# Kernel tuning notes

Measured on AMD Instinct MI355X. Metric: run time of the kernel, lower is better.

## Reference

```python
import jax, jax.numpy as jnp
import numpy as np
import math

def setup_inputs() -> dict:
    key = jax.random.key(0)
    k1, k2, k3 = jax.random.split(key, 3)
    B, N, C = 32, 1024, 768
    x = jax.random.normal(k1, (B, N, C), dtype=jnp.float32)
    W = jax.random.normal(k2, (4, C), dtype=jnp.float32) * 0.02  # conv1x1 weight [out=4, in=C]
    b = jax.random.normal(k3, (4,), dtype=jnp.float32) * 0.02
    return {"x": x, "W": W, "b": b}

def reference(x, W, b):
    B, N, C = x.shape
    H = int(math.isqrt(N))
    L = H * H
    # [B,N,C] -> [B,C,H,H]
    xi = jnp.transpose(x, (0, 2, 1)).reshape(B, C, H, H)
    # alpha = Conv1x1(AvgPool(x)) -> [B,4]
    pooled = jnp.mean(xi, axis=(2, 3))                      # [B,C]
    alpha = pooled @ W.T + b                                # [B,4]
    a = alpha[:, :, None, None]                             # [B,4,1,1]
    # CrossScan directions
    x0 = xi.reshape(B, C, L)                                # row-major scan
    x1 = jnp.transpose(xi, (0, 1, 3, 2)).reshape(B, C, L)   # col-major scan
    x2 = x0[:, :, ::-1]                                     # reversed row-major
    x3 = x1[:, :, ::-1]                                     # reversed col-major
    # gated weighted sum over the 4 scans (fused elementwise)
    y = a[:, 0] * x0 + a[:, 1] * x1 + a[:, 2] * x2 + a[:, 3] * x3  # [B,C,L]
    return jnp.transpose(y, (0, 2, 1))                      # [B,L,C]
```

## Files before the change

kernel.cpp:

```cpp
#include <hip/hip_runtime.h>

#define BB 32
#define NN 1024
#define CC 768
#define HH 32
#define NCHUNK 32
#define NPER (NN / NCHUNK)
#define C4 (CC / 4)

typedef float f32x4 __attribute__((ext_vector_type(4)));

__device__ __forceinline__ f32x4 f4_fma4(float a0, f32x4 v0, float a1, f32x4 v1,
                                         float a2, f32x4 v2, float a3, f32x4 v3) {
    return a0 * v0 + a1 * v1 + a2 * v2 + a3 * v3;
}

__global__ void pool_partial(const f32x4* __restrict__ x4, f32x4* __restrict__ part4) {
    const int blk = blockIdx.x;
    const int b   = blk >> 5;
    const int ch  = blk & 31;
    const int t   = threadIdx.x;
    const f32x4* xb = x4 + ((size_t)(b * NN + ch * NPER)) * C4 + t;
    f32x4 s = {0.f, 0.f, 0.f, 0.f};
#pragma unroll 8
    for (int n = 0; n < NPER; ++n) s += xb[(size_t)n * C4];
    part4[(size_t)blk * C4 + t] = s;
}

__global__ void alpha_kernel(const f32x4* __restrict__ part4,
                             const f32x4* __restrict__ W4,
                             const float* __restrict__ bias,
                             float* __restrict__ alpha) {
    const int b = blockIdx.x;
    const int t = threadIdx.x;
    f32x4 s = {0.f, 0.f, 0.f, 0.f};
#pragma unroll 8
    for (int ch = 0; ch < NCHUNK; ++ch)
        s += part4[((size_t)(b * NCHUNK + ch)) * C4 + t];
    float ak[4];
#pragma unroll
    for (int k = 0; k < 4; ++k) {
        const f32x4 w = W4[k * C4 + t];
        ak[k] = s.x * w.x + s.y * w.y + s.z * w.z + s.w * w.w;
    }
    const int lane = t & 63;
    const int wid  = t >> 6;
    __shared__ float red[3][4];
#pragma unroll
    for (int k = 0; k < 4; ++k) {
        float v = ak[k];
#pragma unroll
        for (int off = 32; off >= 1; off >>= 1) v += __shfl_down(v, off);
        if (lane == 0) red[wid][k] = v;
    }
    __syncthreads();
    if (t < 4) {
        const float s3 = red[0][t] + red[1][t] + red[2][t];
        alpha[b * 4 + t] = s3 * (1.0f / (float)NN) + bias[t];
    }
}

__global__ void merge(const f32x4* __restrict__ x4,
                      const float* __restrict__ alpha,
                      f32x4* __restrict__ o4) {
    const int b = blockIdx.x >> 10;
    const int l = blockIdx.x & 1023;
    const int lt  = ((l & (HH - 1)) << 5) | (l >> 5);
    const int lr  = (NN - 1) - l;
    const int ltr = (NN - 1) - lt;
    if (lt < l || lr < l || ltr < l) return;

    const int t = threadIdx.x;
    const f32x4* xb = x4 + (size_t)b * (NN * C4);
    f32x4* ob = o4 + (size_t)b * (NN * C4);
    const float a0 = alpha[b * 4 + 0];
    const float a1 = alpha[b * 4 + 1];
    const float a2 = alpha[b * 4 + 2];
    const float a3 = alpha[b * 4 + 3];

    const f32x4 v0 = xb[(size_t)l   * C4 + t];
    const f32x4 v1 = xb[(size_t)lt  * C4 + t];
    const f32x4 v2 = xb[(size_t)lr  * C4 + t];
    const f32x4 v3 = xb[(size_t)ltr * C4 + t];

    __builtin_nontemporal_store(f4_fma4(a0, v0, a1, v1, a2, v2, a3, v3), &ob[(size_t)l   * C4 + t]);
    __builtin_nontemporal_store(f4_fma4(a0, v1, a1, v0, a2, v3, a3, v2), &ob[(size_t)lt  * C4 + t]);
    __builtin_nontemporal_store(f4_fma4(a0, v2, a1, v3, a2, v0, a3, v1), &ob[(size_t)lr  * C4 + t]);
    __builtin_nontemporal_store(f4_fma4(a0, v3, a1, v2, a2, v1, a3, v0), &ob[(size_t)ltr * C4 + t]);
}

extern "C" void kernel_launch(void* const* d_in, const int* in_sizes, int n_in,
                              void* d_out, int out_size, void* d_ws, size_t ws_size,
                              hipStream_t stream) {
    const float* x    = (const float*)d_in[0];
    const float* W    = (const float*)d_in[1];
    const float* bias = (const float*)d_in[2];
    float* out = (float*)d_out;

    float* part  = (float*)d_ws;
    float* alpha = part + (size_t)BB * NCHUNK * CC;

    pool_partial<<<BB * NCHUNK, 192, 0, stream>>>((const f32x4*)x, (f32x4*)part);
    alpha_kernel<<<BB, 192, 0, stream>>>((const f32x4*)part, (const f32x4*)W, bias, alpha);
    merge<<<BB * NN, 192, 0, stream>>>((const f32x4*)x, alpha, (f32x4*)out);
}
```

Before: 197.3 us.

## Fold alpha reduction into pool and merge, launch only orbit-representative blocks

```diff
diff --git a/kernel.cpp b/kernel.cpp
--- a/kernel.cpp
+++ b/kernel.cpp
@@ -7,86 +7,89 @@
 #define NCHUNK 32
 #define NPER (NN / NCHUNK)
 #define C4 (CC / 4)
+#define NORB 272
+#define OPB 2
+#define MBLK (NORB / OPB)
 
 typedef float f32x4 __attribute__((ext_vector_type(4)));
 
-__device__ __forceinline__ f32x4 f4_fma4(float a0, f32x4 v0, float a1, f32x4 v1,
-                                         float a2, f32x4 v2, float a3, f32x4 v3) {
-    return a0 * v0 + a1 * v1 + a2 * v2 + a3 * v3;
-}
-
-__global__ void pool_partial(const f32x4* __restrict__ x4, f32x4* __restrict__ part4) {
+__global__ void pool_dot(const f32x4* __restrict__ x4,
+                         const f32x4* __restrict__ W4,
+                         f32x4* __restrict__ partW4) {
     const int blk = blockIdx.x;
-    const int b   = blk >> 5;
-    const int ch  = blk & 31;
     const int t   = threadIdx.x;
-    const f32x4* xb = x4 + ((size_t)(b * NN + ch * NPER)) * C4 + t;
+    const f32x4* xb = x4 + (size_t)blk * (NPER * C4) + t;
     f32x4 s = {0.f, 0.f, 0.f, 0.f};
 #pragma unroll 8
     for (int n = 0; n < NPER; ++n) s += xb[(size_t)n * C4];
-    part4[(size_t)blk * C4 + t] = s;
-}
 
-__global__ void alpha_kernel(const f32x4* __restrict__ part4,
-                             const f32x4* __restrict__ W4,
-                             const float* __restrict__ bias,
-                             float* __restrict__ alpha) {
-    const int b = blockIdx.x;
-    const int t = threadIdx.x;
-    f32x4 s = {0.f, 0.f, 0.f, 0.f};
-#pragma unroll 8
-    for (int ch = 0; ch < NCHUNK; ++ch)
-        s += part4[((size_t)(b * NCHUNK + ch)) * C4 + t];
-    float ak[4];
+    float d[4];
 #pragma unroll
     for (int k = 0; k < 4; ++k) {
         const f32x4 w = W4[k * C4 + t];
-        ak[k] = s.x * w.x + s.y * w.y + s.z * w.z + s.w * w.w;
+        d[k] = s.x * w.x + s.y * w.y + s.z * w.z + s.w * w.w;
     }
     const int lane = t & 63;
     const int wid  = t >> 6;
     __shared__ float red[3][4];
 #pragma unroll
     for (int k = 0; k < 4; ++k) {
-        float v = ak[k];
+        float v = d[k];
 #pragma unroll
         for (int off = 32; off >= 1; off >>= 1) v += __shfl_down(v, off);
         if (lane == 0) red[wid][k] = v;
     }
     __syncthreads();
-    if (t < 4) {
-        const float s3 = red[0][t] + red[1][t] + red[2][t];
-        alpha[b * 4 + t] = s3 * (1.0f / (float)NN) + bias[t];
+    if (t == 0) {
+        f32x4 w;
+        w.x = red[0][0] + red[1][0] + red[2][0];
+        w.y = red[0][1] + red[1][1] + red[2][1];
+        w.z = red[0][2] + red[1][2] + red[2][2];
+        w.w = red[0][3] + red[1][3] + red[2][3];
+        partW4[blk] = w;
     }
 }
 
 __global__ void merge(const f32x4* __restrict__ x4,
-                      const float* __restrict__ alpha,
+                      const f32x4* __restrict__ partW4,
+                      const f32x4* __restrict__ bias4,
                       f32x4* __restrict__ o4) {
-    const int b = blockIdx.x >> 10;
-    const int l = blockIdx.x & 1023;
-    const int lt  = ((l & (HH - 1)) << 5) | (l >> 5);
-    const int lr  = (NN - 1) - l;
-    const int ltr = (NN - 1) - lt;
-    if (lt < l || lr < l || ltr < l) return;
+    const int bidx = blockIdx.x;
+    const int b = bidx / MBLK;
+    const int j = bidx - b * MBLK;
+
+    f32x4 acc = {0.f, 0.f, 0.f, 0.f};
+#pragma unroll 8
+    for (int ch = 0; ch < NCHUNK; ++ch) acc += partW4[b * NCHUNK + ch];
+    const f32x4 al = acc * (1.0f / (float)NN) + bias4[0];
+    const float a0 = al.x, a1 = al.y, a2 = al.z, a3 = al.w;
 
     const int t = threadIdx.x;
     const f32x4* xb = x4 + (size_t)b * (NN * C4);
     f32x4* ob = o4 + (size_t)b * (NN * C4);
-    const float a0 = alpha[b * 4 + 0];
-    const float a1 = alpha[b * 4 + 1];
-    const float a2 = alpha[b * 4 + 2];
-    const float a3 = alpha[b * 4 + 3];
 
-    const f32x4 v0 = xb[(size_t)l   * C4 + t];
-    const f32x4 v1 = xb[(size_t)lt  * C4 + t];
-    const f32x4 v2 = xb[(size_t)lr  * C4 + t];
-    const f32x4 v3 = xb[(size_t)ltr * C4 + t];
+#pragma unroll
+    for (int q = 0; q < OPB; ++q) {
+        const int o = OPB * j + q;
+        int r = 0;
+#pragma unroll
+        for (int rr = 1; rr <= 15; ++rr) if (rr * (33 - rr) <= o) r = rr;
+        const int c = r + (o - r * (33 - r));
+        const int l   = r * HH + c;
+        const int lt  = c * HH + r;
+        const int lr  = (NN - 1) - l;
+        const int ltr = (NN - 1) - lt;
 
-    __builtin_nontemporal_store(f4_fma4(a0, v0, a1, v1, a2, v2, a3, v3), &ob[(size_t)l   * C4 + t]);
-    __builtin_nontemporal_store(f4_fma4(a0, v1, a1, v0, a2, v3, a3, v2), &ob[(size_t)lt  * C4 + t]);
-    __builtin_nontemporal_store(f4_fma4(a0, v2, a1, v3, a2, v0, a3, v1), &ob[(size_t)lr  * C4 + t]);
-    __builtin_nontemporal_store(f4_fma4(a0, v3, a1, v2, a2, v1, a3, v0), &ob[(size_t)ltr * C4 + t]);
+        const f32x4 v0 = xb[(size_t)l   * C4 + t];
+        const f32x4 v1 = xb[(size_t)lt  * C4 + t];
+        const f32x4 v2 = xb[(size_t)lr  * C4 + t];
+        const f32x4 v3 = xb[(size_t)ltr * C4 + t];
+
+        ob[(size_t)l   * C4 + t] = a0 * v0 + a1 * v1 + a2 * v2 + a3 * v3;
+        ob[(size_t)lt  * C4 + t] = a0 * v1 + a1 * v0 + a2 * v3 + a3 * v2;
+        ob[(size_t)lr  * C4 + t] = a0 * v2 + a1 * v3 + a2 * v0 + a3 * v1;
+        ob[(size_t)ltr * C4 + t] = a0 * v3 + a1 * v2 + a2 * v1 + a3 * v0;
+    }
 }
 
 extern "C" void kernel_launch(void* const* d_in, const int* in_sizes, int n_in,
@@ -97,10 +100,9 @@
     const float* bias = (const float*)d_in[2];
     float* out = (float*)d_out;
 
-    float* part  = (float*)d_ws;
-    float* alpha = part + (size_t)BB * NCHUNK * CC;
+    f32x4* partW = (f32x4*)d_ws;
 
-    pool_partial<<<BB * NCHUNK, 192, 0, stream>>>((const f32x4*)x, (f32x4*)part);
-    alpha_kernel<<<BB, 192, 0, stream>>>((const f32x4*)part, (const f32x4*)W, bias, alpha);
-    merge<<<BB * NN, 192, 0, stream>>>((const f32x4*)x, alpha, (f32x4*)out);
+    pool_dot<<<BB * NCHUNK, 192, 0, stream>>>((const f32x4*)x, (const f32x4*)W, partW);
+    merge<<<BB * MBLK, 192, 0, stream>>>((const f32x4*)x, partW,
+                                         (const f32x4*)bias, (f32x4*)out);
 }
```

Result: no change. 195.0 us (-1.2%).
